# Performance work log

Measured on AMD Instinct MI355X. Metric: run time of the kernel, lower is better.

The kernel has to match this reference:

```python
import jax, jax.numpy as jnp
import numpy as np

# Module constants (from init_kwargs)
K = 7        # kernel_size
STRIDE = 1
PAD = 3
B, C, W = 16, 128, 8192


def setup_inputs() -> dict:
    key = jax.random.key(0)
    k1, k2 = jax.random.split(key)
    x = jax.random.normal(k1, (B, C, W), dtype=jnp.float32)
    mask = jax.random.randint(k2, (B, C, W), 0, 20) < 19
    return {"x": x, "mask": mask}


def reference(x, mask):
    # zero out masked values, then reflect-pad x and zero-pad mask
    masked_x = jnp.where(mask, x, jnp.zeros_like(x))
    xp = jnp.pad(masked_x, ((0, 0), (0, 0), (PAD, PAD)), mode="reflect")
    mp = jnp.pad(mask.astype(x.dtype), ((0, 0), (0, 0), (PAD, PAD)))

    # unfold: gather sliding windows  (B, C, n_out, K)
    n_out = (xp.shape[-1] - K) // STRIDE + 1
    win_idx = jnp.arange(n_out)[:, None] * STRIDE + jnp.arange(K)[None, :]
    xw = xp[..., win_idx]
    mw = mp[..., win_idx]

    # masked values -> +inf so they sort to the end
    x_masked = jnp.where(mw.astype(bool), xw, jnp.inf)
    x_sorted = jnp.sort(x_masked, axis=-1)

    valid_count = mw.sum(axis=-1)                      # float, matches torch mask.float().sum
    median_idx = jnp.clip((valid_count - 1) // 2, 0).astype(jnp.int32)
    med = jnp.take_along_axis(x_sorted, median_idx[..., None], axis=-1)[..., 0]

    # windows with zero valid entries -> nan
    return jnp.where(jnp.isinf(med), jnp.nan, med)
```

## Files before the change

kernel.cpp:

```cpp
#include <hip/hip_runtime.h>
#include <math.h>

#define WIDTH 8192
#define NROW  2048
#define T4    (WIDTH / 4)

__global__ void detect_mask_kind(const unsigned* __restrict__ mw,
                                 int* __restrict__ flag) {
    int lid = threadIdx.x;
    int isbyte = 0, isfloat = 0;
#pragma unroll
    for (int j = 0; j < 4; ++j) {
        unsigned w = mw[lid * 4 + j];
        if (w == 0x3F800000u)      isfloat = 1;
        else if (w > 1u)           isbyte  = 1;
    }
    unsigned long long bf = __ballot(isfloat != 0);
    unsigned long long bb = __ballot(isbyte != 0);
    if (lid == 0) flag[0] = bf ? 2 : (bb ? 1 : 0);
}

#define CE(a, b) { float _lo = fminf(a, b); float _hi = fmaxf(a, b); a = _lo; b = _hi; }

__launch_bounds__(256)
__global__ void mmp_kernel(const float* __restrict__ x,
                           const void* __restrict__ mask,
                           const int* __restrict__ flag,
                           float* __restrict__ out) {
    const int bid   = blockIdx.x;
    const int row   = bid >> 3;
    const int chunk = bid & 7;
    const int o0    = chunk * 1024 + threadIdx.x * 4;
    const long base = (long)row * WIDTH;
    const int  t    = o0 >> 2;

    const float4* x4 = (const float4*)x + (base >> 2);
    float4 A  = (t > 0)      ? x4[t - 1] : make_float4(0.f, 0.f, 0.f, 0.f);
    float4 Bv = x4[t];
    float4 Cv = (t < T4 - 1) ? x4[t + 1] : make_float4(0.f, 0.f, 0.f, 0.f);

    unsigned mv = 0;
    const int kind = flag[0];
    if (kind == 0) {
        const int4* m4 = (const int4*)mask + (base >> 2);
        int4 MA = (t > 0)      ? m4[t - 1] : make_int4(0, 0, 0, 0);
        int4 MB = m4[t];
        int4 MC = (t < T4 - 1) ? m4[t + 1] : make_int4(0, 0, 0, 0);
        mv = (unsigned)((MA.x != 0)        | ((MA.y != 0) << 1) |
                        ((MA.z != 0) << 2) | ((MA.w != 0) << 3) |
                        ((MB.x != 0) << 4) | ((MB.y != 0) << 5) |
                        ((MB.z != 0) << 6) | ((MB.w != 0) << 7) |
                        ((MC.x != 0) << 8) | ((MC.y != 0) << 9) |
                        ((MC.z != 0) <<10) | ((MC.w != 0) <<11));
    } else if (kind == 1) {
        const unsigned* mw = (const unsigned*)mask + (base >> 2);
        unsigned wA = (t > 0)      ? mw[t - 1] : 0u;
        unsigned wB = mw[t];
        unsigned wC = (t < T4 - 1) ? mw[t + 1] : 0u;
        mv = (unsigned)(((((wA      ) & 0xFFu) != 0)       ) |
                        ((((wA >> 8) & 0xFFu) != 0) << 1)    |
                        ((((wA >>16) & 0xFFu) != 0) << 2)    |
                        ((((wA >>24) & 0xFFu) != 0) << 3)    |
                        ((((wB      ) & 0xFFu) != 0) << 4)   |
                        ((((wB >> 8) & 0xFFu) != 0) << 5)    |
                        ((((wB >>16) & 0xFFu) != 0) << 6)    |
                        ((((wB >>24) & 0xFFu) != 0) << 7)    |
                        ((((wC      ) & 0xFFu) != 0) << 8)   |
                        ((((wC >> 8) & 0xFFu) != 0) << 9)    |
                        ((((wC >>16) & 0xFFu) != 0) << 10)   |
                        ((((wC >>24) & 0xFFu) != 0) << 11));
    } else {
        const float4* m4 = (const float4*)mask + (base >> 2);
        float4 MA = (t > 0)      ? m4[t - 1] : make_float4(0.f, 0.f, 0.f, 0.f);
        float4 MB = m4[t];
        float4 MC = (t < T4 - 1) ? m4[t + 1] : make_float4(0.f, 0.f, 0.f, 0.f);
        mv = (unsigned)((MA.x != 0.f)        | ((MA.y != 0.f) << 1) |
                        ((MA.z != 0.f) << 2) | ((MA.w != 0.f) << 3) |
                        ((MB.x != 0.f) << 4) | ((MB.y != 0.f) << 5) |
                        ((MB.z != 0.f) << 6) | ((MB.w != 0.f) << 7) |
                        ((MC.x != 0.f) << 8) | ((MC.y != 0.f) << 9) |
                        ((MC.z != 0.f) <<10) | ((MC.w != 0.f) <<11));
    }

    const float xv[12] = { A.x, A.y, A.z, A.w,
                           Bv.x, Bv.y, Bv.z, Bv.w,
                           Cv.x, Cv.y, Cv.z, Cv.w };

    const float INF = __builtin_inff();
    float r0 = 0.f, r1 = 0.f, r2 = 0.f, r3 = 0.f;

#pragma unroll
    for (int i = 0; i < 4; ++i) {
        const unsigned wb = (mv >> (i + 1)) & 0x7Fu;
        const int n = __popc(wb);
        float v0 = (wb & 1u)   ? xv[i + 1] : INF;
        float v1 = (wb & 2u)   ? xv[i + 2] : INF;
        float v2 = (wb & 4u)   ? xv[i + 3] : INF;
        float v3 = (wb & 8u)   ? xv[i + 4] : INF;
        float v4 = (wb & 16u)  ? xv[i + 5] : INF;
        float v5 = (wb & 32u)  ? xv[i + 6] : INF;
        float v6 = (wb & 64u)  ? xv[i + 7] : INF;

#pragma unroll
        for (int rr = 0; rr < 7; ++rr) {
            if ((rr & 1) == 0) { CE(v0, v1); CE(v2, v3); CE(v4, v5); }
            else               { CE(v1, v2); CE(v3, v4); CE(v5, v6); }
        }

        const int k = (n - 1) >> 1;
        float med = (k == 0) ? v0 : (k == 1) ? v1 : (k == 2) ? v2 : v3;
        med = (n == 0) ? __builtin_nanf("") : med;
        if (i == 0) r0 = med; else if (i == 1) r1 = med;
        else if (i == 2) r2 = med; else r3 = med;
    }

    float4* o4 = (float4*)out + (base >> 2);
    o4[t] = make_float4(r0, r1, r2, r3);
}

extern "C" void kernel_launch(void* const* d_in, const int* in_sizes, int n_in,
                              void* d_out, int out_size, void* d_ws, size_t ws_size,
                              hipStream_t stream) {
    const float* x    = (const float*)d_in[0];
    const void*  mask = d_in[1];
    int*   flag = (int*)d_ws;
    float* outp = (float*)d_out;

    detect_mask_kind<<<1, 64, 0, stream>>>((const unsigned*)mask, flag);
    mmp_kernel<<<NROW * 8, 256, 0, stream>>>(x, mask, flag, outp);
}
```

Measured before the change: 50.32 us.

## Compute eight medians per thread with shared sorted sub-networks and merge

Each thread now produces eight outputs instead of four, loading four float4s and reusing shared sorted 4-element blocks plus sorted 3-element tails so that each window median comes from a partial merge rather than a full 7-element odd-even sort. Window counts are updated incrementally. The aim is to cut ALU work per output and lower halo load overhead, at the cost of more registers and half as many blocks.

Measured after the change: 63.86 us. 26.9% more time.

```diff
diff --git a/kernel.cpp b/kernel.cpp
--- a/kernel.cpp
+++ b/kernel.cpp
@@ -20,7 +20,17 @@
     if (lid == 0) flag[0] = bf ? 2 : (bb ? 1 : 0);
 }
 
-#define CE(a, b) { float _lo = fminf(a, b); float _hi = fmaxf(a, b); a = _lo; b = _hi; }
+#define CE(a, b) { float _lo = fminf(a, b); float _hi = fmaxf(a, b); (a) = _lo; (b) = _hi; }
+
+#define MEDIAN(A0,A1,A2,A3, T0,T1,T2, N, DST) {                                   \
+    float _M0 = fminf(A0, T0);                                                    \
+    float _M1 = fminf(fminf(A1, T1), fmaxf(A0, T0));                              \
+    float _M2 = fminf(fminf(A2, T2), fminf(fmaxf(A1, T0), fmaxf(A0, T1)));        \
+    float _M3 = fminf(fminf(A3, fmaxf(A2, T0)),                                   \
+                      fminf(fmaxf(A1, T1), fmaxf(A0, T2)));                       \
+    int   _k  = ((N) - 1) >> 1;                                                   \
+    float _md = (_k <= 0) ? _M0 : (_k == 1) ? _M1 : (_k == 2) ? _M2 : _M3;        \
+    (DST) = (_md == INF) ? __builtin_nanf("") : _md; }
 
 __launch_bounds__(256)
 __global__ void mmp_kernel(const float* __restrict__ x,
@@ -28,94 +38,109 @@
                            const int* __restrict__ flag,
                            float* __restrict__ out) {
     const int bid   = blockIdx.x;
-    const int row   = bid >> 3;
-    const int chunk = bid & 7;
-    const int o0    = chunk * 1024 + threadIdx.x * 4;
-    const long base = (long)row * WIDTH;
-    const int  t    = o0 >> 2;
+    const int row   = bid >> 2;
+    const int chunk = bid & 3;
+    const int o0    = chunk * 2048 + threadIdx.x * 8;
+    const int t     = o0 >> 2;
+    const long rb4  = (long)row * T4;
 
-    const float4* x4 = (const float4*)x + (base >> 2);
-    float4 A  = (t > 0)      ? x4[t - 1] : make_float4(0.f, 0.f, 0.f, 0.f);
-    float4 Bv = x4[t];
-    float4 Cv = (t < T4 - 1) ? x4[t + 1] : make_float4(0.f, 0.f, 0.f, 0.f);
+    const float4* x4 = (const float4*)x + rb4;
+    const float4 Z4  = make_float4(0.f, 0.f, 0.f, 0.f);
+    float4 X0 = (t > 0)      ? x4[t - 1] : Z4;
+    float4 X1 = x4[t];
+    float4 X2 = x4[t + 1];
+    float4 X3 = (t + 2 < T4) ? x4[t + 2] : Z4;
 
-    unsigned mv = 0;
+    const float xv[16] = { X0.x, X0.y, X0.z, X0.w,  X1.x, X1.y, X1.z, X1.w,
+                           X2.x, X2.y, X2.z, X2.w,  X3.x, X3.y, X3.z, X3.w };
+
+    unsigned bv[16];
     const int kind = flag[0];
-    if (kind == 0) {
-        const int4* m4 = (const int4*)mask + (base >> 2);
-        int4 MA = (t > 0)      ? m4[t - 1] : make_int4(0, 0, 0, 0);
-        int4 MB = m4[t];
-        int4 MC = (t < T4 - 1) ? m4[t + 1] : make_int4(0, 0, 0, 0);
-        mv = (unsigned)((MA.x != 0)        | ((MA.y != 0) << 1) |
-                        ((MA.z != 0) << 2) | ((MA.w != 0) << 3) |
-                        ((MB.x != 0) << 4) | ((MB.y != 0) << 5) |
-                        ((MB.z != 0) << 6) | ((MB.w != 0) << 7) |
-                        ((MC.x != 0) << 8) | ((MC.y != 0) << 9) |
-                        ((MC.z != 0) <<10) | ((MC.w != 0) <<11));
-    } else if (kind == 1) {
-        const unsigned* mw = (const unsigned*)mask + (base >> 2);
-        unsigned wA = (t > 0)      ? mw[t - 1] : 0u;
-        unsigned wB = mw[t];
-        unsigned wC = (t < T4 - 1) ? mw[t + 1] : 0u;
-        mv = (unsigned)(((((wA      ) & 0xFFu) != 0)       ) |
-                        ((((wA >> 8) & 0xFFu) != 0) << 1)    |
-                        ((((wA >>16) & 0xFFu) != 0) << 2)    |
-                        ((((wA >>24) & 0xFFu) != 0) << 3)    |
-                        ((((wB      ) & 0xFFu) != 0) << 4)   |
-                        ((((wB >> 8) & 0xFFu) != 0) << 5)    |
-                        ((((wB >>16) & 0xFFu) != 0) << 6)    |
-                        ((((wB >>24) & 0xFFu) != 0) << 7)    |
-                        ((((wC      ) & 0xFFu) != 0) << 8)   |
-                        ((((wC >> 8) & 0xFFu) != 0) << 9)    |
-                        ((((wC >>16) & 0xFFu) != 0) << 10)   |
-                        ((((wC >>24) & 0xFFu) != 0) << 11));
+    if (kind == 1) {
+        const unsigned* mw = (const unsigned*)mask + rb4;
+        unsigned wz[4];
+        wz[0] = (t > 0)      ? mw[t - 1] : 0u;
+        wz[1] = mw[t];
+        wz[2] = mw[t + 1];
+        wz[3] = (t + 2 < T4) ? mw[t + 2] : 0u;
+#pragma unroll
+        for (int j = 1; j <= 14; ++j) {
+            unsigned b = (wz[j >> 2] >> (8 * (j & 3))) & 0xFFu;
+            bv[j] = (b < 1u) ? b : 1u;
+        }
+    } else if (kind == 0) {
+        const int4* m4 = (const int4*)mask + rb4;
+        const int4 ZI = make_int4(0, 0, 0, 0);
+        int4 I0 = (t > 0)      ? m4[t - 1] : ZI;
+        int4 I1 = m4[t];
+        int4 I2 = m4[t + 1];
+        int4 I3 = (t + 2 < T4) ? m4[t + 2] : ZI;
+        const int iv[16] = { I0.x, I0.y, I0.z, I0.w,  I1.x, I1.y, I1.z, I1.w,
+                             I2.x, I2.y, I2.z, I2.w,  I3.x, I3.y, I3.z, I3.w };
+#pragma unroll
+        for (int j = 1; j <= 14; ++j) bv[j] = (iv[j] != 0) ? 1u : 0u;
     } else {
-        const float4* m4 = (const float4*)mask + (base >> 2);
-        float4 MA = (t > 0)      ? m4[t - 1] : make_float4(0.f, 0.f, 0.f, 0.f);
-        float4 MB = m4[t];
-        float4 MC = (t < T4 - 1) ? m4[t + 1] : make_float4(0.f, 0.f, 0.f, 0.f);
-        mv = (unsigned)((MA.x != 0.f)        | ((MA.y != 0.f) << 1) |
-                        ((MA.z != 0.f) << 2) | ((MA.w != 0.f) << 3) |
-                        ((MB.x != 0.f) << 4) | ((MB.y != 0.f) << 5) |
-                        ((MB.z != 0.f) << 6) | ((MB.w != 0.f) << 7) |
-                        ((MC.x != 0.f) << 8) | ((MC.y != 0.f) << 9) |
-                        ((MC.z != 0.f) <<10) | ((MC.w != 0.f) <<11));
+        const float4* m4 = (const float4*)mask + rb4;
+        float4 F0 = (t > 0)      ? m4[t - 1] : Z4;
+        float4 F1 = m4[t];
+        float4 F2 = m4[t + 1];
+        float4 F3 = (t + 2 < T4) ? m4[t + 2] : Z4;
+        const float fv[16] = { F0.x, F0.y, F0.z, F0.w,  F1.x, F1.y, F1.z, F1.w,
+                               F2.x, F2.y, F2.z, F2.w,  F3.x, F3.y, F3.z, F3.w };
+#pragma unroll
+        for (int j = 1; j <= 14; ++j) bv[j] = (fv[j] != 0.f) ? 1u : 0u;
     }
 
-    const float xv[12] = { A.x, A.y, A.z, A.w,
-                           Bv.x, Bv.y, Bv.z, Bv.w,
-                           Cv.x, Cv.y, Cv.z, Cv.w };
+    const float INF = __builtin_inff();
 
-    const float INF = __builtin_inff();
-    float r0 = 0.f, r1 = 0.f, r2 = 0.f, r3 = 0.f;
+    float m[16];
+#pragma unroll
+    for (int j = 1; j <= 14; ++j) m[j] = bv[j] ? xv[j] : INF;
 
-#pragma unroll
-    for (int i = 0; i < 4; ++i) {
-        const unsigned wb = (mv >> (i + 1)) & 0x7Fu;
-        const int n = __popc(wb);
-        float v0 = (wb & 1u)   ? xv[i + 1] : INF;
-        float v1 = (wb & 2u)   ? xv[i + 2] : INF;
-        float v2 = (wb & 4u)   ? xv[i + 3] : INF;
-        float v3 = (wb & 8u)   ? xv[i + 4] : INF;
-        float v4 = (wb & 16u)  ? xv[i + 5] : INF;
-        float v5 = (wb & 32u)  ? xv[i + 6] : INF;
-        float v6 = (wb & 64u)  ? xv[i + 7] : INF;
+    float l23 = m[2],  h23 = m[3];   CE(l23, h23);
+    float l67 = m[6],  h67 = m[7];   CE(l67, h67);
+    float l89 = m[8],  h89 = m[9];   CE(l89, h89);
+    float l1213 = m[12], h1213 = m[13]; CE(l1213, h1213);
 
-#pragma unroll
-        for (int rr = 0; rr < 7; ++rr) {
-            if ((rr & 1) == 0) { CE(v0, v1); CE(v2, v3); CE(v4, v5); }
-            else               { CE(v1, v2); CE(v3, v4); CE(v5, v6); }
-        }
+    float A0 = m[4], A1 = m[5]; CE(A0, A1);
+    float A2 = l67,  A3 = h67;
+    CE(A0, A2); CE(A1, A3); CE(A1, A2);
 
-        const int k = (n - 1) >> 1;
-        float med = (k == 0) ? v0 : (k == 1) ? v1 : (k == 2) ? v2 : v3;
-        med = (n == 0) ? __builtin_nanf("") : med;
-        if (i == 0) r0 = med; else if (i == 1) r1 = med;
-        else if (i == 2) r2 = med; else r3 = med;
-    }
+    float B2 = m[10], B3 = m[11]; CE(B2, B3);
+    float B0 = l89,   B1 = h89;
+    CE(B0, B2); CE(B1, B3); CE(B1, B2);
 
-    float4* o4 = (float4*)out + (base >> 2);
-    o4[t] = make_float4(r0, r1, r2, r3);
+    float u0 = m[1], u1 = l23, u2 = h23;  CE(u0, u1); CE(u1, u2);
+    float v0 = l23,  v1 = h23, v2 = m[8]; CE(v1, v2); CE(v0, v1);
+    float q0 = m[3], q1 = l89, q2 = h89;  CE(q0, q1); CE(q1, q2);
+    float r0 = l89,  r1 = h89, r2 = m[10]; CE(r1, r2); CE(r0, r1);
+    float s0 = m[5], s1 = l67, s2 = h67;  CE(s0, s1); CE(s1, s2);
+    float p0 = l67,  p1 = h67, p2 = m[12]; CE(p1, p2); CE(p0, p1);
+    float g0 = m[7], g1 = l1213, g2 = h1213; CE(g0, g1); CE(g1, g2);
+    float e0 = l1213, e1 = h1213, e2 = m[14]; CE(e1, e2); CE(e0, e1);
+
+    int n0 = (int)(bv[1] + bv[2] + bv[3] + bv[4] + bv[5] + bv[6] + bv[7]);
+    int n1 = n0 - (int)bv[1] + (int)bv[8];
+    int n2 = n1 - (int)bv[2] + (int)bv[9];
+    int n3 = n2 - (int)bv[3] + (int)bv[10];
+    int n4 = n3 - (int)bv[4] + (int)bv[11];
+    int n5 = n4 - (int)bv[5] + (int)bv[12];
+    int n6 = n5 - (int)bv[6] + (int)bv[13];
+    int n7 = n6 - (int)bv[7] + (int)bv[14];
+
+    float o_0, o_1, o_2, o_3, o_4, o_5, o_6, o_7;
+    MEDIAN(A0, A1, A2, A3, u0, u1, u2, n0, o_0);
+    MEDIAN(A0, A1, A2, A3, v0, v1, v2, n1, o_1);
+    MEDIAN(A0, A1, A2, A3, q0, q1, q2, n2, o_2);
+    MEDIAN(A0, A1, A2, A3, r0, r1, r2, n3, o_3);
+    MEDIAN(B0, B1, B2, B3, s0, s1, s2, n4, o_4);
+    MEDIAN(B0, B1, B2, B3, p0, p1, p2, n5, o_5);
+    MEDIAN(B0, B1, B2, B3, g0, g1, g2, n6, o_6);
+    MEDIAN(B0, B1, B2, B3, e0, e1, e2, n7, o_7);
+
+    float4* o4 = (float4*)out + rb4;
+    o4[t]     = make_float4(o_0, o_1, o_2, o_3);
+    o4[t + 1] = make_float4(o_4, o_5, o_6, o_7);
 }
 
 extern "C" void kernel_launch(void* const* d_in, const int* in_sizes, int n_in,
@@ -127,5 +152,5 @@
     float* outp = (float*)d_out;
 
     detect_mask_kind<<<1, 64, 0, stream>>>((const unsigned*)mask, flag);
-    mmp_kernel<<<NROW * 8, 256, 0, stream>>>(x, mask, flag, outp);
+    mmp_kernel<<<NROW * 4, 256, 0, stream>>>(x, mask, flag, outp);
 }
```
